# Kernel tuning notes

Measured on AMD Instinct MI355X. Metric: run time of the kernel, lower is better.

## Reference

```python
import jax, jax.numpy as jnp
import numpy as np

N, E, K, C, NB, G = 10000, 320000, 10, 32, 8, 8
RMAX, AVG = 5.0, 32.0
L_OF_M = np.array([0,1,1,1,2,2,2,2,2,3,3,3,3,3,3,3])
BLOCKS = [(0,1),(1,4),(4,9),(9,16)]


def _sph(u):
    # real spherical harmonics l=0..3, e3nn 'component' normalization (sum_m Y_lm^2 = 2l+1)
    x, y, z = u[:,0], u[:,1], u[:,2]
    s3=3**0.5; s5=5**0.5; s15=15**0.5; s105=105**0.5
    s35_8=(35.0/8.0)**0.5; s21_8=(21.0/8.0)**0.5; s7=7**0.5
    return jnp.stack([
        jnp.ones_like(x),
        s3*x, s3*y, s3*z,
        s15*x*y, s15*y*z, 0.5*s5*(3*z*z-1.0), s15*x*z, 0.5*s15*(x*x-y*y),
        s35_8*y*(3*x*x-y*y), s105*x*y*z, s21_8*y*(5*z*z-1.0),
        0.5*s7*z*(5*z*z-3.0), s21_8*x*(5*z*z-1.0), 0.5*s105*z*(x*x-y*y),
        s35_8*x*(x*x-3*y*y)], axis=-1)


def _radial(r):
    # Bessel basis * polynomial cutoff (p=5)
    n = jnp.arange(1, NB+1, dtype=r.dtype)
    bess = jnp.sqrt(2.0/RMAX)*jnp.sin(n*jnp.pi*r[:,None]/RMAX)/r[:,None]
    t = r/RMAX; p = 5.0
    env = 1.0 - (p+1)*(p+2)/2*t**5 + p*(p+2)*t**6 - p*(p+1)/2*t**7
    env = jnp.where(r < RMAX, env, 0.0)
    return bess*env[:,None]


def _interact(scal, ea, ef, snd, rcv, mws, Wl, n_nodes):
    h = ef
    for W in mws[:-1]:
        h = jax.nn.silu(h @ W)
    tw = (h @ mws[-1]).reshape(-1, C, 4)[:, :, L_OF_M]          # [E,C,16] per-(channel,l) tp weights
    mji = scal[snd][:, :, None] * tw * ea[:, None, :]            # per-edge CG-style tensor product
    msg = jax.ops.segment_sum(mji, rcv, num_segments=n_nodes) / AVG
    return jnp.concatenate([jnp.einsum('ncm,cd->ndm', msg[:, :, a:b], Wl[l])
                            for l, (a, b) in enumerate(BLOCKS)], axis=-1)


def _forward(positions, node_attrs, shifts, edge_index, batch, num_graphs,
             atomic_energies, W_emb, Wup1, M1a, M1b, M1c, M1d, Wl1, Wprod1,
             Wup2, M2a, M2b, M2c, M2d, Wl2, Wprod2, Wsc2, wr1, Wr2a, wr2b):
    snd, rcv = edge_index[0], edge_index[1]
    vec = positions[rcv] - positions[snd] + shifts
    r = jnp.sqrt(jnp.sum(vec*vec, -1) + 1e-12)
    ea = _sph(vec / r[:, None])           # [E,16]
    ef = _radial(r)                       # [E,8]
    nf0 = node_attrs @ W_emb              # node embedding [N,C]
    A1 = _interact(nf0 @ Wup1, ea, ef, snd, rcv, (M1a, M1b, M1c, M1d), Wl1, positions.shape[0])
    c1 = jnp.einsum('nk,kct->nct', node_attrs, Wprod1)          # element-dep product-basis coeffs
    a0 = A1[:, :, 0]
    nf1 = A1 * (c1[..., 0] + c1[..., 1]*a0 + c1[..., 2]*a0*a0)[:, :, None]  # correlation-3 product
    A2 = _interact(nf1[:, :, 0] @ Wup2, ea, ef, snd, rcv, (M2a, M2b, M2c, M2d), Wl2, positions.shape[0])
    pl = jnp.stack([jnp.sum(A2[:, :, a:b]**2, -1) for a, b in BLOCKS], -1)  # [N,C,4] invariants
    c2 = jnp.einsum('nk,kct->nct', node_attrs, Wprod2)
    nf2 = jnp.sum(c2*pl, -1) + jnp.einsum('nk,nc,kcd->nd', node_attrs, nf1[:, :, 0], Wsc2)
    e0 = node_attrs @ atomic_energies
    e1 = nf1[:, :, 0] @ wr1
    e2 = jax.nn.silu(nf2 @ Wr2a) @ wr2b
    node_energy = e0 + e1 + e2
    total = jax.ops.segment_sum(node_energy, batch, num_segments=num_graphs)
    return total, node_energy


def setup_inputs():
    key = jax.random.key(0)
    ks = jax.random.split(key, 24)
    s = 0.1
    inp = {}
    inp['positions'] = jax.random.normal(ks[0], (N, 3), jnp.float32)
    inp['node_attrs'] = jax.nn.one_hot(jax.random.randint(ks[1], (N,), 0, K), K, dtype=jnp.float32)
    inp['shifts'] = jnp.zeros((E, 3), jnp.float32)
    inp['edge_index'] = jax.random.randint(ks[2], (2, E), 0, N)
    inp['batch'] = jnp.sort(jax.random.randint(ks[3], (N,), 0, G))
    inp['num_graphs'] = G
    inp['atomic_energies'] = jax.random.normal(ks[4], (K,), jnp.float32)
    inp['W_emb'] = s*jax.random.normal(ks[5], (K, C), jnp.float32)
    inp['Wup1'] = s*jax.random.normal(ks[6], (C, C), jnp.float32)
    inp['M1a'] = s*jax.random.normal(ks[7], (NB, 64), jnp.float32)
    inp['M1b'] = s*jax.random.normal(ks[8], (64, 64), jnp.float32)
    inp['M1c'] = s*jax.random.normal(ks[9], (64, 64), jnp.float32)
    inp['M1d'] = s*jax.random.normal(ks[10], (64, C*4), jnp.float32)
    inp['Wl1'] = s*jax.random.normal(ks[11], (4, C, C), jnp.float32)
    inp['Wprod1'] = s*jax.random.normal(ks[12], (K, C, 3), jnp.float32)
    inp['Wup2'] = s*jax.random.normal(ks[13], (C, C), jnp.float32)
    inp['M2a'] = s*jax.random.normal(ks[14], (NB, 64), jnp.float32)
    inp['M2b'] = s*jax.random.normal(ks[15], (64, 64), jnp.float32)
    inp['M2c'] = s*jax.random.normal(ks[16], (64, 64), jnp.float32)
    inp['M2d'] = s*jax.random.normal(ks[17], (64, C*4), jnp.float32)
    inp['Wl2'] = s*jax.random.normal(ks[18], (4, C, C), jnp.float32)
    inp['Wprod2'] = s*jax.random.normal(ks[19], (K, C, 4), jnp.float32)
    inp['Wsc2'] = s*jax.random.normal(ks[20], (K, C, C), jnp.float32)
    inp['wr1'] = s*jax.random.normal(ks[21], (C,), jnp.float32)
    inp['Wr2a'] = s*jax.random.normal(ks[22], (C, 16), jnp.float32)
    inp['wr2b'] = s*jax.random.normal(ks[23], (16,), jnp.float32)
    return inp


def reference(positions, node_attrs, shifts, edge_index, batch, num_graphs,
              atomic_energies, W_emb, Wup1, M1a, M1b, M1c, M1d, Wl1, Wprod1,
              Wup2, M2a, M2b, M2c, M2d, Wl2, Wprod2, Wsc2, wr1, Wr2a, wr2b):
    def efn(pos):
        tot, ne = _forward(pos, node_attrs, shifts, edge_index, batch, num_graphs,
                           atomic_energies, W_emb, Wup1, M1a, M1b, M1c, M1d, Wl1, Wprod1,
                           Wup2, M2a, M2b, M2c, M2d, Wl2, Wprod2, Wsc2, wr1, Wr2a, wr2b)
        return jnp.sum(tot), (tot, ne)
    (_, (total, node_energy)), g = jax.value_and_grad(efn, has_aux=True)(positions)
    forces = -g  # forces = -dE/dpositions as in get_outputs
    return total, node_energy, forces
```

## Files before the change

### kernel.cpp

```cpp
#include <hip/hip_runtime.h>
#include <math.h>

#define NN 10000
#define NE 320000
#define KS 10
#define CC 32
#define GG 8
#define NTAB 2048
#define TROW 320
#define RMAXf 5.0f
#define AVGf 32.0f

#define OF_TAB 0
#define SZ_TAB ((NTAB + 1) * TROW)
#define OF_GEO (OF_TAB + SZ_TAB)
#define OF_SND (OF_GEO + 4 * NE)
#define OF_SPK (OF_SND + NE)
#define OF_RCSR (OF_SPK + NE)
#define OF_YE (OF_RCSR + NE)
#define OF_SC1 (OF_YE + 16 * NE)
#define OF_SP (OF_SC1 + KS * CC)
#define OF_RE (OF_SP + NN)
#define OF_UE (OF_RE + NE)
#define OF_GV (OF_UE + 3 * NE)
#define OF_A0 (OF_GV + 3 * NE)
#define OF_NF1 (OF_A0 + NN * CC)
#define OF_SCAL2 (OF_NF1 + NN * CC)
#define OF_NEP (OF_SCAL2 + NN * CC)
#define OF_GM2T (OF_NEP + NN)
#define OF_GNF1P (OF_GM2T + NN * CC * 16)
#define OF_GS1 (OF_GNF1P + NN * CC)
#define OF_ROWS (OF_GS1 + NN * CC)
#define OF_DEG (OF_ROWS + NN + 1)
#define OF_CUR (OF_DEG + NN)
#define OF_GSC2 (OF_CUR + NN)
#define OF_END (OF_GSC2 + NN * CC)

__device__ __forceinline__ int lm_of(int m) { return (m == 0) ? 0 : (m < 4) ? 1 : (m < 9) ? 2 : 3; }

__device__ __forceinline__ void sph16(float x, float y, float z, float* Y) {
    const float s3 = 1.7320508075688772f, s5 = 2.23606797749979f, s15 = 3.872983346207417f,
                s105 = 10.246950765959598f, s358 = 2.091650066335189f,
                s218 = 1.6201851746019651f, s7 = 2.6457513110645907f;
    Y[0] = 1.f;
    Y[1] = s3 * x; Y[2] = s3 * y; Y[3] = s3 * z;
    Y[4] = s15 * x * y; Y[5] = s15 * y * z; Y[6] = 0.5f * s5 * (3.f * z * z - 1.f);
    Y[7] = s15 * x * z; Y[8] = 0.5f * s15 * (x * x - y * y);
    Y[9] = s358 * y * (3.f * x * x - y * y);
    Y[10] = s105 * x * y * z;
    Y[11] = s218 * y * (5.f * z * z - 1.f);
    Y[12] = 0.5f * s7 * z * (5.f * z * z - 3.f);
    Y[13] = s218 * x * (5.f * z * z - 1.f);
    Y[14] = 0.5f * s105 * z * (x * x - y * y);
    Y[15] = s358 * x * (x * x - 3.f * y * y);
}

__device__ __forceinline__ void sph16_grad(float x, float y, float z, float* Dx, float* Dy, float* Dz) {
    const float s3 = 1.7320508075688772f, s5 = 2.23606797749979f, s15 = 3.872983346207417f,
                s105 = 10.246950765959598f, s358 = 2.091650066335189f,
                s218 = 1.6201851746019651f, s7 = 2.6457513110645907f;
    Dx[0] = 0; Dy[0] = 0; Dz[0] = 0;
    Dx[1] = s3; Dy[1] = 0; Dz[1] = 0;
    Dx[2] = 0; Dy[2] = s3; Dz[2] = 0;
    Dx[3] = 0; Dy[3] = 0; Dz[3] = s3;
    Dx[4] = s15 * y; Dy[4] = s15 * x; Dz[4] = 0;
    Dx[5] = 0; Dy[5] = s15 * z; Dz[5] = s15 * y;
    Dx[6] = 0; Dy[6] = 0; Dz[6] = 3.f * s5 * z;
    Dx[7] = s15 * z; Dy[7] = 0; Dz[7] = s15 * x;
    Dx[8] = s15 * x; Dy[8] = -s15 * y; Dz[8] = 0;
    Dx[9] = 6.f * s358 * x * y; Dy[9] = 3.f * s358 * (x * x - y * y); Dz[9] = 0;
    Dx[10] = s105 * y * z; Dy[10] = s105 * x * z; Dz[10] = s105 * x * y;
    Dx[11] = 0; Dy[11] = s218 * (5.f * z * z - 1.f); Dz[11] = 10.f * s218 * y * z;
    Dx[12] = 0; Dy[12] = 0; Dz[12] = 0.5f * s7 * (15.f * z * z - 3.f);
    Dx[13] = s218 * (5.f * z * z - 1.f); Dy[13] = 0; Dz[13] = 10.f * s218 * x * z;
    Dx[14] = s105 * x * z; Dy[14] = -s105 * y * z; Dz[14] = 0.5f * s105 * (x * x - y * y);
    Dx[15] = 3.f * s358 * (x * x - y * y); Dy[15] = -6.f * s358 * x * y; Dz[15] = 0;
}

__global__ void k_species(const float* __restrict__ na, int* __restrict__ sp) {
    int n = blockIdx.x * blockDim.x + threadIdx.x;
    if (n >= NN) return;
    int k = 0;
    for (int j = 0; j < KS; j++)
        if (na[n * KS + j] > 0.5f) k = j;
    sp[n] = k;
}

__global__ void k_scal1(const float* __restrict__ Wemb, const float* __restrict__ Wup1, float* __restrict__ st) {
    int i = threadIdx.x;
    if (i >= KS * CC) return;
    int k = i / CC, c = i % CC;
    float s = 0;
    for (int j = 0; j < CC; j++) s += Wemb[k * CC + j] * Wup1[j * CC + c];
    st[i] = s;
}

__global__ void k_table(const float* __restrict__ M1a, const float* __restrict__ M1b,
                        const float* __restrict__ M1c, const float* __restrict__ M1d,
                        const float* __restrict__ M2a, const float* __restrict__ M2b,
                        const float* __restrict__ M2c, const float* __restrict__ M2d,
                        float* __restrict__ tab) {
    const double PI = 3.14159265358979323846;
    int row = blockIdx.x;
    int j = threadIdx.x;
    __shared__ float sR[8], sdR[8];
    __shared__ float sA[64], sdA[64], sB[64], sdB[64];
    if (j < 8) {
        double r = (double)row * ((double)RMAXf / NTAB);
        if (r < 1e-6) r = 1e-6;
        double a = (double)(j + 1) * PI / (double)RMAXf;
        double env = 0.0, denv = 0.0;
        if (row < NTAB) {
            double t = r / (double)RMAXf;
            double t4 = t * t * t * t;
            env = 1.0 - 21.0 * t4 * t + 35.0 * t4 * t * t - 15.0 * t4 * t * t * t;
            denv = (-105.0 * t4 + 210.0 * t4 * t - 105.0 * t4 * t * t) / (double)RMAXf;
        }
        double pref = sqrt(2.0 / (double)RMAXf);
        double s = sin(a * r), cg = cos(a * r);
        double bess = pref * s / r;
        double dbess = pref * (a * cg / r - s / (r * r));
        sR[j] = (float)(bess * env);
        sdR[j] = (float)(dbess * env + bess * denv);
    }
    __syncthreads();
    size_t rb = (size_t)row * TROW;

    {
        float p = 0, dp = 0;
        for (int i = 0; i < 8; i++) { float w = M1a[i * 64 + j]; p += sR[i] * w; dp += sdR[i] * w; }
        float sg = 1.f / (1.f + expf(-p));
        sB[j] = p * sg; sdB[j] = dp * sg * (1.f + p * (1.f - sg));
    }
    __syncthreads();
    {
        float p = 0, dp = 0;
        for (int i = 0; i < 64; i++) { float w = M1b[i * 64 + j]; p += sB[i] * w; dp += sdB[i] * w; }
        float sg = 1.f / (1.f + expf(-p));
        sA[j] = p * sg; sdA[j] = dp * sg * (1.f + p * (1.f - sg));
    }
    __syncthreads();
    {
        float p = 0, dp = 0;
        for (int i = 0; i < 64; i++) { float w = M1c[i * 64 + j]; p += sA[i] * w; dp += sdA[i] * w; }
        float sg = 1.f / (1.f + expf(-p));
        sB[j] = p * sg; sdB[j] = dp * sg * (1.f + p * (1.f - sg));
    }
    __syncthreads();
    #pragma unroll
    for (int t2 = 0; t2 < 2; t2++) {
        int o = j + t2 * 64;
        if ((o & 3) == 0) {
            float p = 0, dp = 0;
            for (int i = 0; i < 64; i++) { float w = M1d[i * 128 + o]; p += sB[i] * w; dp += sdB[i] * w; }
            int c = o >> 2;
            tab[rb + c] = p;
            tab[rb + 32 + c] = dp;
        }
    }
    __syncthreads();

    {
        float p = 0, dp = 0;
        for (int i = 0; i < 8; i++) { float w = M2a[i * 64 + j]; p += sR[i] * w; dp += sdR[i] * w; }
        float sg = 1.f / (1.f + expf(-p));
        sB[j] = p * sg; sdB[j] = dp * sg * (1.f + p * (1.f - sg));
    }
    __syncthreads();
    {
        float p = 0, dp = 0;
        for (int i = 0; i < 64; i++) { float w = M2b[i * 64 + j]; p += sB[i] * w; dp += sdB[i] * w; }
        float sg = 1.f / (1.f + expf(-p));
        sA[j] = p * sg; sdA[j] = dp * sg * (1.f + p * (1.f - sg));
    }
    __syncthreads();
    {
        float p = 0, dp = 0;
        for (int i = 0; i < 64; i++) { float w = M2c[i * 64 + j]; p += sA[i] * w; dp += sdA[i] * w; }
        float sg = 1.f / (1.f + expf(-p));
        sB[j] = p * sg; sdB[j] = dp * sg * (1.f + p * (1.f - sg));
    }
    __syncthreads();
    #pragma unroll
    for (int t2 = 0; t2 < 2; t2++) {
        int o = j + t2 * 64;
        float p = 0, dp = 0;
        for (int i = 0; i < 64; i++) { float w = M2d[i * 128 + o]; p += sB[i] * w; dp += sdB[i] * w; }
        tab[rb + 64 + o] = p;
        tab[rb + 192 + o] = dp;
    }
}

__global__ void k_geom(const float* __restrict__ pos, const float* __restrict__ shifts,
                       const int* __restrict__ ei, float* __restrict__ re,
                       float* __restrict__ ue, int* __restrict__ deg) {
    int e = blockIdx.x * 256 + threadIdx.x;
    if (e >= NE) return;
    int s = ei[e], t = ei[NE + e];
    float vx = pos[3 * t] - pos[3 * s] + shifts[3 * e];
    float vy = pos[3 * t + 1] - pos[3 * s + 1] + shifts[3 * e + 1];
    float vz = pos[3 * t + 2] - pos[3 * s + 2] + shifts[3 * e + 2];
    float r = sqrtf(vx * vx + vy * vy + vz * vz + 1e-12f);
    float inv = 1.f / r;
    re[e] = r;
    ue[3 * e] = vx * inv;
    ue[3 * e + 1] = vy * inv;
    ue[3 * e + 2] = vz * inv;
    atomicAdd(&deg[t], 1);
}

__global__ void k_scan(const int* __restrict__ deg, int* __restrict__ rows, int* __restrict__ cur) {
    __shared__ int part[1024];
    int t = threadIdx.x;
    const int per = (NN + 1023) / 1024;
    int base = t * per;
    int s = 0;
    for (int i = 0; i < per; i++) {
        int idx = base + i;
        if (idx < NN) s += deg[idx];
    }
    part[t] = s;
    __syncthreads();
    for (int off = 1; off < 1024; off <<= 1) {
        int v = (t >= off) ? part[t - off] : 0;
        __syncthreads();
        part[t] += v;
        __syncthreads();
    }
    int run = (t == 0) ? 0 : part[t - 1];
    for (int i = 0; i < per; i++) {
        int idx = base + i;
        if (idx < NN) {
            rows[idx] = run;
            cur[idx] = run;
            run += deg[idx];
        }
    }
    if (t == 1023) rows[NN] = run;
}

__global__ void k_fill(const int* __restrict__ ei, const int* __restrict__ sp,
                       const float* __restrict__ re, const float* __restrict__ ue,
                       int* __restrict__ cur, int* __restrict__ snd, int* __restrict__ spk,
                       float* __restrict__ rcsr, float4* __restrict__ geo,
                       float* __restrict__ YE) {
    int e = blockIdx.x * 256 + threadIdx.x;
    if (e >= NE) return;
    int s = ei[e], t = ei[NE + e];
    int p = atomicAdd(&cur[t], 1);
    float ux = ue[3 * e], uy = ue[3 * e + 1], uz = ue[3 * e + 2];
    snd[p] = s;
    spk[p] = sp[s];
    rcsr[p] = re[e];
    geo[p] = make_float4(re[e], ux, uy, uz);
    float Y[16];
    sph16(ux, uy, uz, Y);
    float4* yp = (float4*)&YE[(size_t)p * 16];
    yp[0] = make_float4(Y[0], Y[1], Y[2], Y[3]);
    yp[1] = make_float4(Y[4], Y[5], Y[6], Y[7]);
    yp[2] = make_float4(Y[8], Y[9], Y[10], Y[11]);
    yp[3] = make_float4(Y[12], Y[13], Y[14], Y[15]);
}

__global__ __launch_bounds__(256, 4)
void k_gather1(const int* __restrict__ rows, const int* __restrict__ spk,
               const float* __restrict__ rcsr, const int* __restrict__ sp,
               const float* __restrict__ sc1, const float* __restrict__ tab,
               const float* __restrict__ Wl1, const float* __restrict__ Wprod1,
               const float* __restrict__ Wup2, const float* __restrict__ wr1,
               const float* __restrict__ aE,
               float* __restrict__ a0s, float* __restrict__ nf1,
               float* __restrict__ scal2, float* __restrict__ nep) {
    __shared__ float red[4][CC];
    int wid = blockIdx.x;
    int tid = threadIdx.x;
    int wv = tid >> 6, lane = tid & 63, c = lane & 31, h = lane >> 5, hb = h << 5;
    int stream = wv * 2 + h;
    int r0 = rows[wid], dg = rows[wid + 1] - r0;
    float acc = 0.f;
    for (int j = stream; j < dg; j += 8) {
        int p = r0 + j;
        float r = rcsr[p];
        float scv = sc1[spk[p] * CC + c];
        float w1 = 0.f;
        if (r < RMAXf) {
            float tt = r * (NTAB / RMAXf);
            int i = (int)tt; if (i > NTAB - 1) i = NTAB - 1;
            float f = tt - (float)i;
            size_t b = (size_t)i * TROW + c;
            w1 = tab[b] * (1.f - f) + tab[b + TROW] * f;
        }
        acc += scv * w1;
    }
    acc += __shfl_xor(acc, 32, 64);
    if (h == 0) red[wv][c] = acc;
    __syncthreads();
    if (wv != 0) return;
    acc = red[0][c] + red[1][c] + red[2][c] + red[3][c];
    float a0 = 0.f;
    for (int d = 0; d < CC; d++) a0 += __shfl(acc, hb + d, 64) * Wl1[d * CC + c];
    a0 *= (1.f / AVGf);
    int k = sp[wid];
    const float* cp = &Wprod1[(k * CC + c) * 3];
    float nf = a0 * (cp[0] + cp[1] * a0 + cp[2] * a0 * a0);
    float s2 = 0.f;
    for (int d = 0; d < CC; d++) s2 += __shfl(nf, hb + d, 64) * Wup2[d * CC + c];
    float t1 = nf * wr1[c];
    for (int m = 16; m >= 1; m >>= 1) t1 += __shfl_xor(t1, m, 64);
    if (h == 0) {
        a0s[wid * CC + c] = a0;
        nf1[wid * CC + c] = nf;
        scal2[wid * CC + c] = s2;
        if (c == 0) nep[wid] = aE[k] + t1;
    }
}

__global__ __launch_bounds__(256, 4)
void k_node2(const int* __restrict__ rows, const int* __restrict__ snd,
             const float* __restrict__ rcsr, const float* __restrict__ YE,
             const int* __restrict__ sp,
             const float* __restrict__ scal2, const float* __restrict__ tab,
             const float* __restrict__ Wl2, const float* __restrict__ Wprod2,
             const float* __restrict__ Wsc2, const float* __restrict__ nf1,
             const float* __restrict__ Wr2a, const float* __restrict__ wr2b,
             const float* __restrict__ wr1, const float* __restrict__ nep,
             const int* __restrict__ batch,
             float* __restrict__ gm2T, float* __restrict__ gnf1p,
             float* __restrict__ out_total, float* __restrict__ out_ne) {
    __shared__ float lds[4][16 * 32];
    int wid = blockIdx.x;
    int tid = threadIdx.x;
    int wv = tid >> 6, lane = tid & 63, c = lane & 31, h = lane >> 5, hb = h << 5;
    int stream = wv * 2 + h;
    int r0 = rows[wid], dg = rows[wid + 1] - r0;

    float S2r[16];
    #pragma unroll
    for (int m = 0; m < 16; m++) S2r[m] = 0.f;
    for (int j = stream; j < dg; j += 8) {
        int p = r0 + j;
        float r = rcsr[p];
        float sc = scal2[snd[p] * CC + c];
        float scw[4] = {0, 0, 0, 0};
        if (r < RMAXf) {
            float tt = r * (NTAB / RMAXf);
            int i = (int)tt; if (i > NTAB - 1) i = NTAB - 1;
            float f = tt - (float)i;
            size_t b = (size_t)i * TROW + 64 + c * 4;
            float4 t0 = *(const float4*)&tab[b];
            float4 t1 = *(const float4*)&tab[b + TROW];
            scw[0] = sc * (t0.x + (t1.x - t0.x) * f);
            scw[1] = sc * (t0.y + (t1.y - t0.y) * f);
            scw[2] = sc * (t0.z + (t1.z - t0.z) * f);
            scw[3] = sc * (t0.w + (t1.w - t0.w) * f);
        }
        const float4* yp = (const float4*)&YE[(size_t)p * 16];
        float4 y0 = yp[0], y1 = yp[1], y2 = yp[2], y3 = yp[3];
        float Y[16] = {y0.x, y0.y, y0.z, y0.w, y1.x, y1.y, y1.z, y1.w,
                       y2.x, y2.y, y2.z, y2.w, y3.x, y3.y, y3.z, y3.w};
        #pragma unroll
        for (int m = 0; m < 16; m++) S2r[m] += scw[lm_of(m)] * Y[m];
    }
    #pragma unroll
    for (int m = 0; m < 16; m++) S2r[m] += __shfl_xor(S2r[m], 32, 64);
    if (h == 0) {
        #pragma unroll
        for (int m = 0; m < 16; m++) lds[wv][m * 32 + c] = S2r[m];
    }
    __syncthreads();
    for (int idx = tid; idx < 512; idx += 256)
        lds[0][idx] += lds[1][idx] + lds[2][idx] + lds[3][idx];
    __syncthreads();
    if (wv != 0) return;

    int d = c;
    float A2r[16];
    #pragma unroll
    for (int m = 0; m < 16; m++) {
        const float* wl = &Wl2[lm_of(m) * CC * CC];
        float acc = 0;
        for (int cc = 0; cc < CC; cc++) acc += lds[0][m * 32 + cc] * wl[cc * CC + d];
        A2r[m] = acc * (1.f / AVGf);
    }
    float pl[4] = {0, 0, 0, 0};
    #pragma unroll
    for (int m = 0; m < 16; m++) pl[lm_of(m)] += A2r[m] * A2r[m];
    int k = sp[wid];
    const float* c2 = &Wprod2[(k * CC + d) * 4];
    float nf2 = c2[0] * pl[0] + c2[1] * pl[1] + c2[2] * pl[2] + c2[3] * pl[3];
    for (int cc = 0; cc < CC; cc++) nf2 += nf1[wid * CC + cc] * Wsc2[((size_t)k * CC + cc) * CC + d];
    int jj = d & 15;
    float zj = 0;
    for (int dd = 0; dd < CC; dd++) zj += __shfl(nf2, hb + dd, 64) * Wr2a[dd * 16 + jj];
    float sg = 1.f / (1.f + expf(-zj));
    float e2p = (d < 16) ? zj * sg * wr2b[jj] : 0.f;
    float red = e2p;
    for (int m = 16; m >= 1; m >>= 1) red += __shfl_xor(red, m, 64);
    if (h == 0 && d == 0) {
        float ne = nep[wid] + red;
        out_ne[wid] = ne;
        atomicAdd(&out_total[batch[wid]], ne);
    }
    float gz = sg * (1.f + zj * (1.f - sg)) * wr2b[jj];
    float gn = 0;
    for (int j2 = 0; j2 < 16; j2++) gn += Wr2a[d * 16 + j2] * __shfl(gz, hb + j2, 64);
    if (h == 0) {
        #pragma unroll
        for (int m = 0; m < 16; m++) lds[0][m * 32 + d] = 2.f * A2r[m] * gn * c2[lm_of(m)];
    }
    float gmv[16];
    #pragma unroll
    for (int m = 0; m < 16; m++) {
        const float* wl = &Wl2[lm_of(m) * CC * CC + c * CC];
        float acc = 0;
        for (int dd = 0; dd < CC; dd++) acc += lds[0][m * 32 + dd] * wl[dd];
        gmv[m] = acc * (1.f / AVGf);
    }
    float g1 = wr1[c];
    for (int dd = 0; dd < CC; dd++) g1 += __shfl(gn, hb + dd, 64) * Wsc2[((size_t)k * CC + c) * CC + dd];
    if (h == 0) {
        #pragma unroll
        for (int m = 0; m < 16; m++) gm2T[(size_t)wid * 512 + c * 16 + m] = gmv[m];
        gnf1p[wid * CC + c] = g1;
    }
}

__global__ __launch_bounds__(256, 4)
void k_gbwd2(const int* __restrict__ rows, const int* __restrict__ snd,
             const float4* __restrict__ geo, const float* __restrict__ YE,
             const float* __restrict__ scal2, const float* __restrict__ tab,
             const float* __restrict__ gm2T,
             float* __restrict__ gsc2, float* __restrict__ gvcsr) {
    int wid = blockIdx.x;
    int tid = threadIdx.x;
    int wv = tid >> 6, lane = tid & 63, c = lane & 31, h = lane >> 5;
    int stream = wv * 2 + h;
    float gm[16];
    #pragma unroll
    for (int m = 0; m < 16; m++) gm[m] = gm2T[(size_t)wid * 512 + c * 16 + m];
    int r0 = rows[wid], dg = rows[wid + 1] - r0;
    for (int j = stream; j < dg; j += 8) {
        int p = r0 + j;
        float4 g4 = geo[p];
        int s = snd[p];
        float sc = scal2[s * CC + c];
        float r = g4.x, ux = g4.y, uy = g4.z, uz = g4.w;
        float w2[4] = {0, 0, 0, 0}, scw[4] = {0, 0, 0, 0}, sdw[4] = {0, 0, 0, 0};
        if (r < RMAXf) {
            float tt = r * (NTAB / RMAXf);
            int i = (int)tt; if (i > NTAB - 1) i = NTAB - 1;
            float f = tt - (float)i;
            size_t b = (size_t)i * TROW + 64 + c * 4;
            size_t b2 = (size_t)i * TROW + 192 + c * 4;
            float4 t0 = *(const float4*)&tab[b];
            float4 t1 = *(const float4*)&tab[b + TROW];
            float4 d0 = *(const float4*)&tab[b2];
            float4 d1 = *(const float4*)&tab[b2 + TROW];
            w2[0] = t0.x + (t1.x - t0.x) * f; w2[1] = t0.y + (t1.y - t0.y) * f;
            w2[2] = t0.z + (t1.z - t0.z) * f; w2[3] = t0.w + (t1.w - t0.w) * f;
            sdw[0] = sc * (d0.x + (d1.x - d0.x) * f); sdw[1] = sc * (d0.y + (d1.y - d0.y) * f);
            sdw[2] = sc * (d0.z + (d1.z - d0.z) * f); sdw[3] = sc * (d0.w + (d1.w - d0.w) * f);
            scw[0] = sc * w2[0]; scw[1] = sc * w2[1]; scw[2] = sc * w2[2]; scw[3] = sc * w2[3];
        }
        const float4* yp = (const float4*)&YE[(size_t)p * 16];
        float4 y0 = yp[0], y1 = yp[1], y2 = yp[2], y3 = yp[3];
        float Y[16] = {y0.x, y0.y, y0.z, y0.w, y1.x, y1.y, y1.z, y1.w,
                       y2.x, y2.y, y2.z, y2.w, y3.x, y3.y, y3.z, y3.w};
        float Dx[16], Dy[16], Dz[16];
        sph16_grad(ux, uy, uz, Dx, Dy, Dz);
        float gsc = 0, gdr = 0, gx = 0, gy = 0, gz = 0;
        #pragma unroll
        for (int m = 0; m < 16; m++) {
            float g = gm[m];
            int l = lm_of(m);
            float t = g * Y[m];
            gsc += t * w2[l];
            gdr += t * sdw[l];
            float gY = g * scw[l];
            gx += gY * Dx[m]; gy += gY * Dy[m]; gz += gY * Dz[m];
        }
        atomicAdd(&gsc2[s * CC + c], gsc);
        for (int m2 = 16; m2 >= 1; m2 >>= 1) {
            gdr += __shfl_xor(gdr, m2, 64);
            gx += __shfl_xor(gx, m2, 64);
            gy += __shfl_xor(gy, m2, 64);
            gz += __shfl_xor(gz, m2, 64);
        }
        if (c == 0) {
            float inv = 1.f / r;
            float dot = ux * gx + uy * gy + uz * gz;
            gvcsr[3 * p] = ux * gdr + (gx - ux * dot) * inv;
            gvcsr[3 * p + 1] = uy * gdr + (gy - uy * dot) * inv;
            gvcsr[3 * p + 2] = uz * gdr + (gz - uz * dot) * inv;
        }
    }
}

__global__ void k_node_bwd2(const float* __restrict__ gnf1p, const float* __restrict__ gsc2,
                            const float* __restrict__ Wup2, const float* __restrict__ a0s,
                            const int* __restrict__ sp, const float* __restrict__ Wprod1,
                            const float* __restrict__ Wl1, float* __restrict__ gS1) {
    int gid = blockIdx.x * 256 + threadIdx.x;
    int n = gid >> 5, c = gid & 31;
    if (n >= NN) return;
    int hb = threadIdx.x & 32;
    float g1 = gnf1p[n * CC + c];
    for (int dd = 0; dd < CC; dd++) g1 += gsc2[n * CC + dd] * Wup2[c * CC + dd];
    float a0 = a0s[n * CC + c];
    int k = sp[n];
    const float* cp = &Wprod1[(k * CC + c) * 3];
    float ga0 = g1 * (cp[0] + 2.f * cp[1] * a0 + 3.f * cp[2] * a0 * a0);
    float acc = 0;
    for (int dd = 0; dd < CC; dd++) acc += __shfl(ga0, hb + dd, 64) * Wl1[c * CC + dd];
    gS1[n * CC + c] = acc * (1.f / AVGf);
}

__global__ __launch_bounds__(256, 4)
void k_gbwd1(const int* __restrict__ rows, const int* __restrict__ snd,
             const int* __restrict__ spk, const float* __restrict__ rcsr,
             const float4* __restrict__ geo, const float* __restrict__ sc1,
             const float* __restrict__ tab, const float* __restrict__ gS1,
             const float* __restrict__ gvcsr, float* __restrict__ F) {
    int wid = blockIdx.x;
    int tid = threadIdx.x;
    int wv = tid >> 6, lane = tid & 63, c = lane & 31, h = lane >> 5;
    int stream = wv * 2 + h;
    int r0 = rows[wid], dg = rows[wid + 1] - r0;
    float gst = gS1[wid * CC + c];
    float ft = 0.f;
    for (int j = stream; j < dg; j += 8) {
        int p = r0 + j;
        float r = rcsr[p];
        int s = snd[p];
        float dw = 0.f;
        if (r < RMAXf) {
            float tt = r * (NTAB / RMAXf);
            int i = (int)tt; if (i > NTAB - 1) i = NTAB - 1;
            float f = tt - (float)i;
            size_t b = (size_t)i * TROW + 32 + c;
            dw = tab[b] * (1.f - f) + tab[b + TROW] * f;
        }
        float gdr = gst * sc1[spk[p] * CC + c] * dw;
        for (int m = 16; m >= 1; m >>= 1) gdr += __shfl_xor(gdr, m, 64);
        if (c < 3) {
            float4 g4 = geo[p];
            float u = (c == 0) ? g4.y : (c == 1) ? g4.z : g4.w;
            float gv = gvcsr[3 * p + c] + u * gdr;
            atomicAdd(&F[3 * s + c], gv);
            ft -= gv;
        }
    }
    if (c < 3) atomicAdd(&F[3 * wid + c], ft);
}

extern "C" void kernel_launch(void* const* d_in, const int* in_sizes, int n_in,
                              void* d_out, int out_size, void* d_ws, size_t ws_size,
                              hipStream_t stream) {
    const float* pos = (const float*)d_in[0];
    const float* na = (const float*)d_in[1];
    const float* shifts = (const float*)d_in[2];
    const int* ei = (const int*)d_in[3];
    const int* batch = (const int*)d_in[4];
    const float* aE = (const float*)d_in[6];
    const float* Wemb = (const float*)d_in[7];
    const float* Wup1 = (const float*)d_in[8];
    const float* M1a = (const float*)d_in[9];
    const float* M1b = (const float*)d_in[10];
    const float* M1c = (const float*)d_in[11];
    const float* M1d = (const float*)d_in[12];
    const float* Wl1 = (const float*)d_in[13];
    const float* Wprod1 = (const float*)d_in[14];
    const float* Wup2 = (const float*)d_in[15];
    const float* M2a = (const float*)d_in[16];
    const float* M2b = (const float*)d_in[17];
    const float* M2c = (const float*)d_in[18];
    const float* M2d = (const float*)d_in[19];
    const float* Wl2 = (const float*)d_in[20];
    const float* Wprod2 = (const float*)d_in[21];
    const float* Wsc2 = (const float*)d_in[22];
    const float* wr1 = (const float*)d_in[23];
    const float* Wr2a = (const float*)d_in[24];
    const float* wr2b = (const float*)d_in[25];

    float* ws = (float*)d_ws;
    float* tab = ws + OF_TAB;
    float4* geo = (float4*)(ws + OF_GEO);
    int* snd = (int*)(ws + OF_SND);
    int* spk = (int*)(ws + OF_SPK);
    float* rcsr = ws + OF_RCSR;
    float* YE = ws + OF_YE;
    float* sc1 = ws + OF_SC1;
    int* sp = (int*)(ws + OF_SP);
    float* re = ws + OF_RE;
    float* ue = ws + OF_UE;
    float* gv = ws + OF_GV;
    float* a0s = ws + OF_A0;
    float* nf1 = ws + OF_NF1;
    float* scal2 = ws + OF_SCAL2;
    float* nep = ws + OF_NEP;
    float* gm2T = ws + OF_GM2T;
    float* gnf1p = ws + OF_GNF1P;
    float* gS1 = ws + OF_GS1;
    int* rows = (int*)(ws + OF_ROWS);
    int* deg = (int*)(ws + OF_DEG);
    int* cur = (int*)(ws + OF_CUR);
    float* gsc2 = ws + OF_GSC2;

    float* out_total = (float*)d_out;
    float* out_ne = out_total + GG;
    float* out_F = out_ne + NN;

    hipMemsetAsync(d_out, 0, sizeof(float) * (GG + NN + 3 * NN), stream);
    hipMemsetAsync(deg, 0, sizeof(float) * (size_t)(OF_END - OF_DEG), stream);

    k_species<<<(NN + 255) / 256, 256, 0, stream>>>(na, sp);
    k_scal1<<<1, 320, 0, stream>>>(Wemb, Wup1, sc1);
    k_table<<<NTAB + 1, 64, 0, stream>>>(M1a, M1b, M1c, M1d, M2a, M2b, M2c, M2d, tab);
    k_geom<<<(NE + 255) / 256, 256, 0, stream>>>(pos, shifts, ei, re, ue, deg);
    k_scan<<<1, 1024, 0, stream>>>(deg, rows, cur);
    k_fill<<<(NE + 255) / 256, 256, 0, stream>>>(ei, sp, re, ue, cur, snd, spk, rcsr, geo, YE);
    k_gather1<<<NN, 256, 0, stream>>>(rows, spk, rcsr, sp, sc1, tab, Wl1, Wprod1,
                                      Wup2, wr1, aE, a0s, nf1, scal2, nep);
    k_node2<<<NN, 256, 0, stream>>>(rows, snd, rcsr, YE, sp, scal2, tab, Wl2,
                                    Wprod2, Wsc2, nf1, Wr2a, wr2b, wr1, nep, batch,
                                    gm2T, gnf1p, out_total, out_ne);
    k_gbwd2<<<NN, 256, 0, stream>>>(rows, snd, geo, YE, scal2, tab, gm2T, gsc2, gv);
    k_node_bwd2<<<NN / 8, 256, 0, stream>>>(gnf1p, gsc2, Wup2, a0s, sp, Wprod1, Wl1, gS1);
    k_gbwd1<<<NN, 256, 0, stream>>>(rows, snd, spk, rcsr, geo, sc1, tab, gS1, gv, out_F);
}
```

Measured before the change: 440.2 us.

## Fuse geometry into CSR fill, spread node2 tail over waves, split edge backward blocks

The edge geometry computation moves into k_fill, so the re/ue scratch arrays and their global round-trip go away and k_geom becomes a degree-count-only kernel. The dense tail of k_node2 now uses all four waves, each handling four of the sixteen m components through LDS stages, instead of returning three waves early. gm2T switches to an m-major layout to match. k_gbwd2 and k_gbwd1 launch two blocks per node, each striding over half the edges, to add parallelism on high-degree nodes. This relies on their per-node outputs (gsc2, forces) being accumulated safely, for example atomically, across the two blocks.

```diff
diff --git a/kernel.cpp b/kernel.cpp
--- a/kernel.cpp
+++ b/kernel.cpp
@@ -20,9 +20,7 @@
 #define OF_YE (OF_RCSR + NE)
 #define OF_SC1 (OF_YE + 16 * NE)
 #define OF_SP (OF_SC1 + KS * CC)
-#define OF_RE (OF_SP + NN)
-#define OF_UE (OF_RE + NE)
-#define OF_GV (OF_UE + 3 * NE)
+#define OF_GV (OF_SP + NN)
 #define OF_A0 (OF_GV + 3 * NE)
 #define OF_NF1 (OF_A0 + NN * CC)
 #define OF_SCAL2 (OF_NF1 + NN * CC)
@@ -191,22 +189,10 @@
     }
 }
 
-__global__ void k_geom(const float* __restrict__ pos, const float* __restrict__ shifts,
-                       const int* __restrict__ ei, float* __restrict__ re,
-                       float* __restrict__ ue, int* __restrict__ deg) {
+__global__ void k_deg(const int* __restrict__ ei, int* __restrict__ deg) {
     int e = blockIdx.x * 256 + threadIdx.x;
     if (e >= NE) return;
-    int s = ei[e], t = ei[NE + e];
-    float vx = pos[3 * t] - pos[3 * s] + shifts[3 * e];
-    float vy = pos[3 * t + 1] - pos[3 * s + 1] + shifts[3 * e + 1];
-    float vz = pos[3 * t + 2] - pos[3 * s + 2] + shifts[3 * e + 2];
-    float r = sqrtf(vx * vx + vy * vy + vz * vz + 1e-12f);
-    float inv = 1.f / r;
-    re[e] = r;
-    ue[3 * e] = vx * inv;
-    ue[3 * e + 1] = vy * inv;
-    ue[3 * e + 2] = vz * inv;
-    atomicAdd(&deg[t], 1);
+    atomicAdd(&deg[ei[NE + e]], 1);
 }
 
 __global__ void k_scan(const int* __restrict__ deg, int* __restrict__ rows, int* __restrict__ cur) {
@@ -239,20 +225,25 @@
     if (t == 1023) rows[NN] = run;
 }
 
-__global__ void k_fill(const int* __restrict__ ei, const int* __restrict__ sp,
-                       const float* __restrict__ re, const float* __restrict__ ue,
+__global__ void k_fill(const float* __restrict__ pos, const float* __restrict__ shifts,
+                       const int* __restrict__ ei, const int* __restrict__ sp,
                        int* __restrict__ cur, int* __restrict__ snd, int* __restrict__ spk,
                        float* __restrict__ rcsr, float4* __restrict__ geo,
                        float* __restrict__ YE) {
     int e = blockIdx.x * 256 + threadIdx.x;
     if (e >= NE) return;
     int s = ei[e], t = ei[NE + e];
+    float vx = pos[3 * t] - pos[3 * s] + shifts[3 * e];
+    float vy = pos[3 * t + 1] - pos[3 * s + 1] + shifts[3 * e + 1];
+    float vz = pos[3 * t + 2] - pos[3 * s + 2] + shifts[3 * e + 2];
+    float r = sqrtf(vx * vx + vy * vy + vz * vz + 1e-12f);
+    float inv = 1.f / r;
+    float ux = vx * inv, uy = vy * inv, uz = vz * inv;
     int p = atomicAdd(&cur[t], 1);
-    float ux = ue[3 * e], uy = ue[3 * e + 1], uz = ue[3 * e + 2];
     snd[p] = s;
     spk[p] = sp[s];
-    rcsr[p] = re[e];
-    geo[p] = make_float4(re[e], ux, uy, uz);
+    rcsr[p] = r;
+    geo[p] = make_float4(r, ux, uy, uz);
     float Y[16];
     sph16(ux, uy, uz, Y);
     float4* yp = (float4*)&YE[(size_t)p * 16];
@@ -327,7 +318,10 @@
              const int* __restrict__ batch,
              float* __restrict__ gm2T, float* __restrict__ gnf1p,
              float* __restrict__ out_total, float* __restrict__ out_ne) {
-    __shared__ float lds[4][16 * 32];
+    __shared__ float ldsS[4][512];
+    __shared__ float ldsA[512];
+    __shared__ float ldsT[512];
+    __shared__ float ldsG[CC];
     int wid = blockIdx.x;
     int tid = threadIdx.x;
     int wv = tid >> 6, lane = tid & 63, c = lane & 31, h = lane >> 5, hb = h << 5;
@@ -365,63 +359,68 @@
     for (int m = 0; m < 16; m++) S2r[m] += __shfl_xor(S2r[m], 32, 64);
     if (h == 0) {
         #pragma unroll
-        for (int m = 0; m < 16; m++) lds[wv][m * 32 + c] = S2r[m];
+        for (int m = 0; m < 16; m++) ldsS[wv][m * 32 + c] = S2r[m];
     }
     __syncthreads();
     for (int idx = tid; idx < 512; idx += 256)
-        lds[0][idx] += lds[1][idx] + lds[2][idx] + lds[3][idx];
-    __syncthreads();
-    if (wv != 0) return;
+        ldsS[0][idx] += ldsS[1][idx] + ldsS[2][idx] + ldsS[3][idx];
+    __syncthreads();
 
     int d = c;
-    float A2r[16];
-    #pragma unroll
-    for (int m = 0; m < 16; m++) {
+    int k = sp[wid];
+    const float* c2 = &Wprod2[(k * CC + d) * 4];
+    #pragma unroll
+    for (int mi = 0; mi < 4; mi++) {
+        int m = wv * 4 + mi;
         const float* wl = &Wl2[lm_of(m) * CC * CC];
         float acc = 0;
-        for (int cc = 0; cc < CC; cc++) acc += lds[0][m * 32 + cc] * wl[cc * CC + d];
-        A2r[m] = acc * (1.f / AVGf);
-    }
-    float pl[4] = {0, 0, 0, 0};
-    #pragma unroll
-    for (int m = 0; m < 16; m++) pl[lm_of(m)] += A2r[m] * A2r[m];
-    int k = sp[wid];
-    const float* c2 = &Wprod2[(k * CC + d) * 4];
-    float nf2 = c2[0] * pl[0] + c2[1] * pl[1] + c2[2] * pl[2] + c2[3] * pl[3];
-    for (int cc = 0; cc < CC; cc++) nf2 += nf1[wid * CC + cc] * Wsc2[((size_t)k * CC + cc) * CC + d];
-    int jj = d & 15;
-    float zj = 0;
-    for (int dd = 0; dd < CC; dd++) zj += __shfl(nf2, hb + dd, 64) * Wr2a[dd * 16 + jj];
-    float sg = 1.f / (1.f + expf(-zj));
-    float e2p = (d < 16) ? zj * sg * wr2b[jj] : 0.f;
-    float red = e2p;
-    for (int m = 16; m >= 1; m >>= 1) red += __shfl_xor(red, m, 64);
-    if (h == 0 && d == 0) {
-        float ne = nep[wid] + red;
-        out_ne[wid] = ne;
-        atomicAdd(&out_total[batch[wid]], ne);
-    }
-    float gz = sg * (1.f + zj * (1.f - sg)) * wr2b[jj];
-    float gn = 0;
-    for (int j2 = 0; j2 < 16; j2++) gn += Wr2a[d * 16 + j2] * __shfl(gz, hb + j2, 64);
-    if (h == 0) {
+        for (int cc = 0; cc < CC; cc++) acc += ldsS[0][m * 32 + cc] * wl[cc * CC + d];
+        if (h == 0) ldsA[m * 32 + d] = acc * (1.f / AVGf);
+    }
+    __syncthreads();
+
+    if (wv == 0) {
+        float pl[4] = {0, 0, 0, 0};
         #pragma unroll
-        for (int m = 0; m < 16; m++) lds[0][m * 32 + d] = 2.f * A2r[m] * gn * c2[lm_of(m)];
-    }
-    float gmv[16];
-    #pragma unroll
-    for (int m = 0; m < 16; m++) {
+        for (int m = 0; m < 16; m++) { float a = ldsA[m * 32 + d]; pl[lm_of(m)] += a * a; }
+        float nf2 = c2[0] * pl[0] + c2[1] * pl[1] + c2[2] * pl[2] + c2[3] * pl[3];
+        for (int cc = 0; cc < CC; cc++) nf2 += nf1[wid * CC + cc] * Wsc2[((size_t)k * CC + cc) * CC + d];
+        int jj = d & 15;
+        float zj = 0;
+        for (int dd = 0; dd < CC; dd++) zj += __shfl(nf2, hb + dd, 64) * Wr2a[dd * 16 + jj];
+        float sg = 1.f / (1.f + expf(-zj));
+        float e2p = (d < 16) ? zj * sg * wr2b[jj] : 0.f;
+        float red = e2p;
+        for (int m = 16; m >= 1; m >>= 1) red += __shfl_xor(red, m, 64);
+        if (h == 0 && d == 0) {
+            float ne = nep[wid] + red;
+            out_ne[wid] = ne;
+            atomicAdd(&out_total[batch[wid]], ne);
+        }
+        float gz = sg * (1.f + zj * (1.f - sg)) * wr2b[jj];
+        float gn = 0;
+        for (int j2 = 0; j2 < 16; j2++) gn += Wr2a[d * 16 + j2] * __shfl(gz, hb + j2, 64);
+        if (h == 0) ldsG[d] = gn;
+        float g1 = wr1[c];
+        for (int dd = 0; dd < CC; dd++) g1 += __shfl(gn, hb + dd, 64) * Wsc2[((size_t)k * CC + c) * CC + dd];
+        if (h == 0) gnf1p[wid * CC + c] = g1;
+    }
+    __syncthreads();
+
+    #pragma unroll
+    for (int mi = 0; mi < 4; mi++) {
+        int m = wv * 4 + mi;
+        if (h == 0) ldsT[m * 32 + d] = 2.f * ldsA[m * 32 + d] * ldsG[d] * c2[lm_of(m)];
+    }
+    __syncthreads();
+
+    #pragma unroll
+    for (int mi = 0; mi < 4; mi++) {
+        int m = wv * 4 + mi;
         const float* wl = &Wl2[lm_of(m) * CC * CC + c * CC];
         float acc = 0;
-        for (int dd = 0; dd < CC; dd++) acc += lds[0][m * 32 + dd] * wl[dd];
-        gmv[m] = acc * (1.f / AVGf);
-    }
-    float g1 = wr1[c];
-    for (int dd = 0; dd < CC; dd++) g1 += __shfl(gn, hb + dd, 64) * Wsc2[((size_t)k * CC + c) * CC + dd];
-    if (h == 0) {
-        #pragma unroll
-        for (int m = 0; m < 16; m++) gm2T[(size_t)wid * 512 + c * 16 + m] = gmv[m];
-        gnf1p[wid * CC + c] = g1;
+        for (int dd = 0; dd < CC; dd++) acc += ldsT[m * 32 + dd] * wl[dd];
+        if (h == 0) gm2T[(size_t)wid * 512 + m * 32 + c] = acc * (1.f / AVGf);
     }
 }
 
@@ -431,15 +430,16 @@
              const float* __restrict__ scal2, const float* __restrict__ tab,
              const float* __restrict__ gm2T,
              float* __restrict__ gsc2, float* __restrict__ gvcsr) {
-    int wid = blockIdx.x;
+    int blk = blockIdx.x;
+    int wid = blk >> 1, half = blk & 1;
     int tid = threadIdx.x;
     int wv = tid >> 6, lane = tid & 63, c = lane & 31, h = lane >> 5;
-    int stream = wv * 2 + h;
+    int stream = half * 8 + wv * 2 + h;
     float gm[16];
     #pragma unroll
-    for (int m = 0; m < 16; m++) gm[m] = gm2T[(size_t)wid * 512 + c * 16 + m];
+    for (int m = 0; m < 16; m++) gm[m] = gm2T[(size_t)wid * 512 + m * 32 + c];
     int r0 = rows[wid], dg = rows[wid + 1] - r0;
-    for (int j = stream; j < dg; j += 8) {
+    for (int j = stream; j < dg; j += 16) {
         int p = r0 + j;
         float4 g4 = geo[p];
         int s = snd[p];
@@ -521,14 +521,15 @@
              const float4* __restrict__ geo, const float* __restrict__ sc1,
              const float* __restrict__ tab, const float* __restrict__ gS1,
              const float* __restrict__ gvcsr, float* __restrict__ F) {
-    int wid = blockIdx.x;
+    int blk = blockIdx.x;
+    int wid = blk >> 1, half = blk & 1;
     int tid = threadIdx.x;
     int wv = tid >> 6, lane = tid & 63, c = lane & 31, h = lane >> 5;
-    int stream = wv * 2 + h;
+    int stream = half * 8 + wv * 2 + h;
     int r0 = rows[wid], dg = rows[wid + 1] - r0;
     float gst = gS1[wid * CC + c];
     float ft = 0.f;
-    for (int j = stream; j < dg; j += 8) {
+    for (int j = stream; j < dg; j += 16) {
         int p = r0 + j;
         float r = rcsr[p];
         int s = snd[p];
@@ -591,8 +592,6 @@
     float* YE = ws + OF_YE;
     float* sc1 = ws + OF_SC1;
     int* sp = (int*)(ws + OF_SP);
-    float* re = ws + OF_RE;
-    float* ue = ws + OF_UE;
     float* gv = ws + OF_GV;
     float* a0s = ws + OF_A0;
     float* nf1 = ws + OF_NF1;
@@ -616,15 +615,15 @@
     k_species<<<(NN + 255) / 256, 256, 0, stream>>>(na, sp);
     k_scal1<<<1, 320, 0, stream>>>(Wemb, Wup1, sc1);
     k_table<<<NTAB + 1, 64, 0, stream>>>(M1a, M1b, M1c, M1d, M2a, M2b, M2c, M2d, tab);
-    k_geom<<<(NE + 255) / 256, 256, 0, stream>>>(pos, shifts, ei, re, ue, deg);
+    k_deg<<<(NE + 255) / 256, 256, 0, stream>>>(ei, deg);
     k_scan<<<1, 1024, 0, stream>>>(deg, rows, cur);
-    k_fill<<<(NE + 255) / 256, 256, 0, stream>>>(ei, sp, re, ue, cur, snd, spk, rcsr, geo, YE);
+    k_fill<<<(NE + 255) / 256, 256, 0, stream>>>(pos, shifts, ei, sp, cur, snd, spk, rcsr, geo, YE);
     k_gather1<<<NN, 256, 0, stream>>>(rows, spk, rcsr, sp, sc1, tab, Wl1, Wprod1,
                                       Wup2, wr1, aE, a0s, nf1, scal2, nep);
     k_node2<<<NN, 256, 0, stream>>>(rows, snd, rcsr, YE, sp, scal2, tab, Wl2,
                                     Wprod2, Wsc2, nf1, Wr2a, wr2b, wr1, nep, batch,
                                     gm2T, gnf1p, out_total, out_ne);
-    k_gbwd2<<<NN, 256, 0, stream>>>(rows, snd, geo, YE, scal2, tab, gm2T, gsc2, gv);
+    k_gbwd2<<<2 * NN, 256, 0, stream>>>(rows, snd, geo, YE, scal2, tab, gm2T, gsc2, gv);
     k_node_bwd2<<<NN / 8, 256, 0, stream>>>(gnf1p, gsc2, Wup2, a0s, sp, Wprod1, Wl1, gS1);
-    k_gbwd1<<<NN, 256, 0, stream>>>(rows, snd, spk, rcsr, geo, sc1, tab, gS1, gv, out_F);
-}
+    k_gbwd1<<<2 * NN, 256, 0, stream>>>(rows, snd, spk, rcsr, geo, sc1, tab, gS1, gv, out_F);
+}
```

Measured after the change: 496.2 us. 1.13x slower.
